# Kernel tuning notes

Measured on AMD Instinct MI355X. Metric: run time of the kernel, lower is better.

## Reference

```python
import jax, jax.numpy as jnp
import numpy as np

B, T, C = 2, 2048, 2048
H, KV, D = 16, 4, 128   # n_head, n_kv_head, head_dim
EPS = 1.1920929e-07     # torch.finfo(float32).eps, F.rms_norm default


def setup_inputs() -> dict:
    key = jax.random.key(0)
    ks = jax.random.split(key, 7)
    x = jax.random.normal(ks[0], (B, T, C), dtype=jnp.float32)
    # rope angles: cos/sin of positions, broadcastable to [B,T,H,D//2]
    inv_freq = 1.0 / (10000.0 ** (jnp.arange(0, D // 2, dtype=jnp.float32) / (D // 2)))
    ang = jnp.arange(T, dtype=jnp.float32)[:, None] * inv_freq[None, :]
    cos = jnp.cos(ang)[None, :, None, :]  # [1,T,1,D/2]
    sin = jnp.sin(ang)[None, :, None, :]
    s = 0.02
    Wq = jax.random.normal(ks[1], (C, H * D), dtype=jnp.float32) * s
    Wk = jax.random.normal(ks[2], (C, KV * D), dtype=jnp.float32) * s
    Wv = jax.random.normal(ks[3], (C, KV * D), dtype=jnp.float32) * s
    Wo = jax.random.normal(ks[4], (C, C), dtype=jnp.float32) * s
    return {"x": x, "cos": cos, "sin": sin, "Wq": Wq, "Wk": Wk, "Wv": Wv, "Wo": Wo}


def _rope(t, cos, sin):
    d = t.shape[-1] // 2
    t1, t2 = t[..., :d], t[..., d:]
    return jnp.concatenate([t1 * cos + t2 * sin, -t1 * sin + t2 * cos], axis=-1)


def _rmsnorm(t):
    return t * jax.lax.rsqrt(jnp.mean(t * t, axis=-1, keepdims=True) + EPS)


def reference(x, cos, sin, Wq, Wk, Wv, Wo):
    q = (x @ Wq).reshape(B, T, H, D)
    k = (x @ Wk).reshape(B, T, KV, D)
    v = (x @ Wv).reshape(B, T, KV, D)
    q = _rmsnorm(_rope(q, cos, sin))
    k = _rmsnorm(_rope(k, cos, sin))
    # [B, KV, G, T, D] query grouped per kv head (GQA)
    G = H // KV
    qh = q.transpose(0, 2, 1, 3).reshape(B, KV, G, T, D)
    kh = k.transpose(0, 2, 1, 3)  # [B, KV, T, D]
    vh = v.transpose(0, 2, 1, 3)
    scale = 1.0 / np.sqrt(D).astype(np.float32)
    scores = jnp.einsum('bhgqd,bhkd->bhgqk', qh, kh) * scale
    causal = jnp.tril(jnp.ones((T, T), dtype=bool))
    scores = jnp.where(causal, scores, jnp.finfo(scores.dtype).min)
    attn = jax.nn.softmax(scores, axis=-1)
    y = jnp.einsum('bhgqk,bhkd->bhgqd', attn, vh)  # [B,KV,G,T,D]
    y = y.reshape(B, H, T, D).transpose(0, 2, 1, 3).reshape(B, T, C)
    return y @ Wo
```

## Files before the change

kernel.cpp:

```cpp
#include <hip/hip_runtime.h>

using bf16x8 = __attribute__((ext_vector_type(8))) short;
using f32x4  = __attribute__((ext_vector_type(4))) float;

#define B_  2
#define T_  2048
#define C_  2048
#define H_  16
#define KV_ 4
#define D_  128

__device__ __forceinline__ unsigned short f2b(float f) {
  union { float f; unsigned int u; } v; v.f = f;
  unsigned int r = v.u + 0x7fffu + ((v.u >> 16) & 1u);
  return (unsigned short)(r >> 16);
}
__device__ __forceinline__ float b2f(unsigned short u) {
  union { unsigned int u; float f; } v; v.u = ((unsigned int)u) << 16;
  return v.f;
}
__device__ __forceinline__ unsigned int cvt_pk_bf16(float lo, float hi) {
  unsigned int r;
  asm("v_cvt_pk_bf16_f32 %0, %1, %2" : "=v"(r) : "v"(lo), "v"(hi));
  return r;
}
__device__ __forceinline__ void gld_lds16(const void* g, void* l) {
  __builtin_amdgcn_global_load_lds(
      (__attribute__((address_space(1))) void*)g,
      (__attribute__((address_space(3))) void*)l, 16, 0, 0);
}

__global__ void cast_bf16_k(const float* __restrict__ in, unsigned short* __restrict__ out) {
  int i = blockIdx.x * 256 + threadIdx.x;
  float4 f = ((const float4*)in)[i];
  ushort4 u; u.x = f2b(f.x); u.y = f2b(f.y); u.z = f2b(f.z); u.w = f2b(f.w);
  ((ushort4*)out)[i] = u;
}

__global__ void wtrans4(const float* __restrict__ Wq, const float* __restrict__ Wk,
                        const float* __restrict__ Wv, const float* __restrict__ Wo,
                        unsigned short* __restrict__ Wqt, unsigned short* __restrict__ Wkt,
                        unsigned short* __restrict__ Wvt, unsigned short* __restrict__ Wot) {
  __shared__ float s[32][33];
  int id = blockIdx.x;
  const float* W; unsigned short* Wt; int N;
  if (id < 4096)      { W = Wq; Wt = Wqt; N = 2048; }
  else if (id < 5120) { W = Wk; Wt = Wkt; N = 512;  id -= 4096; }
  else if (id < 6144) { W = Wv; Wt = Wvt; N = 512;  id -= 5120; }
  else                { W = Wo; Wt = Wot; N = 2048; id -= 6144; }
  int ntiles = N >> 5;
  int n0 = (id % ntiles) * 32, k0 = (id / ntiles) * 32;
  int tx = threadIdx.x, ty = threadIdx.y;
  #pragma unroll
  for (int yy = 0; yy < 32; yy += 8)
    s[ty + yy][tx] = W[(size_t)(k0 + ty + yy) * N + n0 + tx];
  __syncthreads();
  #pragma unroll
  for (int yy = 0; yy < 32; yy += 8)
    Wt[(size_t)(n0 + ty + yy) * 2048 + k0 + tx] = f2b(s[tx][ty + yy]);
}

template <bool OUT_BF16>
__device__ __forceinline__ void gemm_tile(
    const unsigned short* __restrict__ A, const unsigned short* __restrict__ Bt,
    void* __restrict__ Cv, int K, int ldc, int m0, int n0b, int n0c,
    unsigned short* sA, unsigned short* sB)
{
  const int tid  = threadIdx.x;
  const int lane = tid & 63, w = tid >> 6;
  const int quad = lane >> 4, l16 = lane & 15;
  const int wm = (w >> 1) * 64, wn = (w & 1) * 64;

  f32x4 acc[4][4] = {};

  const unsigned short* Abase = A  + (size_t)m0  * K;
  const unsigned short* Bbase = Bt + (size_t)n0b * K;

  for (int k0 = 0; k0 < K; k0 += 32) {
    #pragma unroll
    for (int r = 0; r < 2; ++r) {
      int c = tid + r * 256;
      int row = c >> 2, col = (c & 3) * 8;
      gld_lds16(Abase + (size_t)row * K + k0 + col, sA + c * 8);
      gld_lds16(Bbase + (size_t)row * K + k0 + col, sB + c * 8);
    }
    __syncthreads();
    bf16x8 af[4], bfr[4];
    #pragma unroll
    for (int i = 0; i < 4; ++i)
      af[i]  = *(const bf16x8*)(sA + (wm + i * 16 + l16) * 32 + quad * 8);
    #pragma unroll
    for (int j = 0; j < 4; ++j)
      bfr[j] = *(const bf16x8*)(sB + (wn + j * 16 + l16) * 32 + quad * 8);
    #pragma unroll
    for (int i = 0; i < 4; ++i)
      #pragma unroll
      for (int j = 0; j < 4; ++j)
        acc[i][j] = __builtin_amdgcn_mfma_f32_16x16x32_bf16(af[i], bfr[j], acc[i][j], 0, 0, 0);
    __syncthreads();
  }
  #pragma unroll
  for (int i = 0; i < 4; ++i) {
    #pragma unroll
    for (int r = 0; r < 4; ++r) {
      int row = m0 + wm + i * 16 + quad * 4 + r;
      #pragma unroll
      for (int j = 0; j < 4; ++j) {
        int col = n0c + wn + j * 16 + l16;
        float v = acc[i][j][r];
        if (OUT_BF16) ((unsigned short*)Cv)[(size_t)row * ldc + col] = f2b(v);
        else          ((float*)Cv)[(size_t)row * ldc + col] = v;
      }
    }
  }
}

__global__ void out_gemm(const unsigned short* __restrict__ yb,
                         const unsigned short* __restrict__ Wot,
                         float* __restrict__ out) {
  __shared__ unsigned short sA[128 * 32], sB[128 * 32];
  gemm_tile<false>(yb, Wot, out, C_, C_, blockIdx.y * 128, blockIdx.x * 128, blockIdx.x * 128,
                   sA, sB);
}

__global__ __launch_bounds__(512, 2) void qkv_gemm2p(
    const unsigned short* __restrict__ xb,
    const unsigned short* __restrict__ Wt,
    unsigned short* __restrict__ qkv) {
  __shared__ unsigned short lds[57344];

  const int id  = (int)blockIdx.x;
  const int xcd = id & 7, j = id >> 3;
  const int mt  = xcd * 2 + (j >> 4);
  const int nt  = j & 15;
  const int m0 = mt * 256, n0 = nt * 192;

  const int tid = (int)threadIdx.x;
  const int w = tid >> 6, lane = tid & 63;
  const int quad = lane >> 4, l16 = lane & 15;
  const int wr = w >> 1, wc = w & 1;
  const int swz = (l16 & 12) << 1;

  const unsigned short* Ab = xb + (size_t)m0 * 2048;
  const unsigned short* Bb = Wt + (size_t)n0 * 2048;

  int ar[4], axc[4];
  #pragma unroll
  for (int kq = 0; kq < 4; ++kq) {
    int ca = tid + kq * 512;
    ar[kq]  = (ca & 1023) >> 2;
    axc[kq] = ((ca & 3) * 8) ^ ((((ca & 1023) >> 4) & 3) << 3);
  }
  const int khb1 = (tid < 256) ? 0 : 1;
  int bidx[3] = { tid, tid + 512 - khb1 * 768, tid + 256 };
  int bkh[3]  = { 0, khb1, 1 };
  int br[3], bxc[3];
  #pragma unroll
  for (int kq = 0; kq < 3; ++kq) {
    br[kq]  = bidx[kq] >> 2;
    bxc[kq] = ((bidx[kq] & 3) * 8) ^ (((bidx[kq] >> 4) & 3) << 3);
  }

#define STAGE(buf, kb) do { \
    unsigned short* da_ = lds + (buf) * 16384; \
    _Pragma("unroll") \
    for (int kq = 0; kq < 4; ++kq) { \
      int ca_ = tid + kq * 512; \
      gld_lds16(Ab + (size_t)ar[kq] * 2048 + (kb) + (ca_ >> 10) * 32 + axc[kq], da_ + ca_ * 8); \
    } \
    unsigned short* db_ = lds + 32768 + (buf) * 12288; \
    _Pragma("unroll") \
    for (int kq = 0; kq < 3; ++kq) \
      gld_lds16(Bb + (size_t)br[kq] * 2048 + (kb) + bkh[kq] * 32 + bxc[kq], \
                db_ + bkh[kq] * 6144 + bidx[kq] * 8); \
  } while (0)

  f32x4 acc[4][6] = {};

  STAGE(0, 0);
  __syncthreads();

  const unsigned short* aB = lds + (wr * 64 + l16) * 32 + (quad * 8 ^ swz);
  const unsigned short* bB = lds + 32768 + (wc * 96 + l16) * 32 + (quad * 8 ^ swz);

  for (int t = 0; t < 32; ++t) {
    const int cur = t & 1;
    if (t < 31) STAGE(cur ^ 1, (t + 1) * 64);
    #pragma unroll
    for (int kh = 0; kh < 2; ++kh) {
      bf16x8 a[4], b[6];
      #pragma unroll
      for (int m = 0; m < 4; ++m)
        a[m] = *(const bf16x8*)(aB + cur * 16384 + kh * 8192 + m * 512);
      #pragma unroll
      for (int n = 0; n < 6; ++n)
        b[n] = *(const bf16x8*)(bB + cur * 12288 + kh * 6144 + n * 512);
      #pragma unroll
      for (int m = 0; m < 4; ++m)
        #pragma unroll
        for (int n = 0; n < 6; ++n)
          acc[m][n] = __builtin_amdgcn_mfma_f32_16x16x32_bf16(a[m], b[n], acc[m][n], 0, 0, 0);
    }
    __syncthreads();
  }
#undef STAGE

  #pragma unroll
  for (int m = 0; m < 4; ++m)
    #pragma unroll
    for (int r = 0; r < 4; ++r) {
      int row = m0 + wr * 64 + m * 16 + quad * 4 + r;
      #pragma unroll
      for (int n = 0; n < 6; ++n) {
        int col = n0 + wc * 96 + n * 16 + l16;
        qkv[(size_t)row * 3072 + col] = f2b(acc[m][n][r]);
      }
    }
}

template <int NH>
__global__ void ropenorm(const unsigned short* __restrict__ in,
                         const float* __restrict__ cs, const float* __restrict__ sn,
                         unsigned short* __restrict__ out, float oscale, int ld, int off) {
  int row  = blockIdx.x * 4 + (threadIdx.x >> 6);
  int lane = threadIdx.x & 63;
  int head = row % NH;
  int t = (row / NH) & (T_ - 1);
  int b = row / (NH * T_);
  const unsigned short* p = in + (size_t)(b * T_ + t) * ld + off + head * D_;
  unsigned int u  = *(const unsigned int*)(p + 2 * lane);
  unsigned int up = (unsigned int)__shfl_xor((int)u, 32, 64);
  int dh = (lane & 31) * 2;
  float2 c2 = ((const float2*)(cs + t * 64))[lane & 31];
  float2 s2 = ((const float2*)(sn + t * 64))[lane & 31];
  float a0 = b2f((unsigned short)(u & 0xffff)),  a1 = b2f((unsigned short)(u >> 16));
  float p0 = b2f((unsigned short)(up & 0xffff)), p1 = b2f((unsigned short)(up >> 16));
  float sgn = (lane < 32) ? 1.0f : -1.0f;
  float oa = a0 * c2.x + sgn * p0 * s2.x;
  float ob = a1 * c2.y + sgn * p1 * s2.y;
  float ss = oa * oa + ob * ob;
  #pragma unroll
  for (int off2 = 32; off2 > 0; off2 >>= 1) ss += __shfl_xor(ss, off2, 64);
  float r = rsqrtf(ss * (1.0f / 128.0f) + 1.1920929e-07f) * oscale;
  unsigned int outu = cvt_pk_bf16(oa * r, ob * r);
  size_t base = ((size_t)((b * NH + head) * 128 + (t >> 4))) * 2048 + (size_t)(t & 15) * 8;
  int f = ((lane < 32) ? 0 : 8) + (dh >> 3);
  *(unsigned int*)(out + base + (size_t)f * 128 + (dh & 7)) = outu;
}

__global__ void vfrag_k(const unsigned short* __restrict__ qkv, unsigned short* __restrict__ vf) {
  int it = blockIdx.x;
  int b = blockIdx.y >> 2, kv = blockIdx.y & 3;
  int d = threadIdx.x, ty = threadIdx.y;
  int t0 = it * 64;
  size_t obase = ((size_t)((b * KV_ + kv) * 32 + it)) * 8192
               + (size_t)(d >> 4) * 1024 + (size_t)(d & 15) * 8;
  #pragma unroll
  for (int tcg = 0; tcg < 4; ++tcg) {
    int tc = ty * 4 + tcg;
    unsigned short val[8];
    #pragma unroll
    for (int e = 0; e < 8; ++e)
      val[e] = qkv[((size_t)(b * T_) + t0 + tc * 8 + e) * 3072 + 2560 + kv * D_ + d];
    ushort4 u0 = {val[0], val[1], val[2], val[3]};
    ushort4 u1 = {val[4], val[5], val[6], val[7]};
    *(ushort4*)(vf + obase + (size_t)tc * 128)     = u0;
    *(ushort4*)(vf + obase + (size_t)tc * 128 + 4) = u1;
  }
}

__global__ __launch_bounds__(512, 2) void attn_kernel(
    const unsigned short* __restrict__ qf, const unsigned short* __restrict__ kf,
    const unsigned short* __restrict__ vf, unsigned short* __restrict__ yb) {
  __shared__ __align__(16) char smem[135168];
  unsigned short* kls = (unsigned short*)smem;
  unsigned short* vls = (unsigned short*)(smem + 65536);
  unsigned short* Pls = (unsigned short*)(smem + 98304);

  const int xp = (int)blockIdx.x, b = xp >> 2, kv = xp & 3;
  const int jy = (int)blockIdx.y;
  const int tid = (int)threadIdx.x;
  const int w = tid >> 6, lane = tid & 63;
  const int quad = lane >> 4, l16 = lane & 15;
  const int hh = w & 3, half = w >> 2;
  const int h = kv * 4 + hh;
  unsigned short* myP = Pls + w * (32 * 72);

  const unsigned short* Kf = kf + (size_t)(b * KV_ + kv) * 128 * 2048;
  const unsigned short* Vf = vf + (size_t)(b * KV_ + kv) * 32 * 8192;

  const int swl = quad << 4;
  const int cs0 = (tid * 8) ^ swl;
  const int cs1 = ((tid + 512) * 8) ^ swl;
  const int cd0 = tid * 8, cd1 = tid * 8 + 4096;

#define STAGE_K(buf, it0) do { \
    const unsigned short* s_ = Kf + (size_t)(it0) * 8192; \
    unsigned short* d_ = kls + (buf) * 16384; \
    gld_lds16(s_ + cs0, d_ + cd0);               gld_lds16(s_ + cs1, d_ + cd1); \
    gld_lds16(s_ + 8192 + cs0, d_ + 8192 + cd0); gld_lds16(s_ + 8192 + cs1, d_ + 8192 + cd1); \
  } while (0)
#define STAGE_V(it0) do { \
    const unsigned short* s_ = Vf + (size_t)(it0) * 8192; \
    gld_lds16(s_ + cs0, vls + cd0);               gld_lds16(s_ + cs1, vls + cd1); \
    gld_lds16(s_ + 8192 + cs0, vls + 8192 + cd0); gld_lds16(s_ + 8192 + cs1, vls + 8192 + cd1); \
  } while (0)

  for (int ph = 0; ph < 2; ++ph) {
    const int qt = ph ? (63 - jy) : jy;
    const int q0 = qt * 32;
    const int ntile = (qt >> 1) + 1;
    const int R = (ntile + 1) >> 1;

    const unsigned short* Qf = qf + ((size_t)(b * H_ + h) * 128 + qt * 2) * 2048;
    bf16x8 bq[2][4];
    #pragma unroll
    for (int i = 0; i < 2; ++i)
      #pragma unroll
      for (int kk = 0; kk < 4; ++kk)
        bq[i][kk] = *(const bf16x8*)(Qf + (size_t)i * 2048 + (kk * 4 + quad) * 128 + l16 * 8);

    float l_i[2] = {0.f, 0.f};
    f32x4 o[2][8] = {};

    STAGE_K(0, 0);

    for (int r = 0; r < R; ++r) {
      const int cur = r & 1;
      const bool more = (r + 1 < R);
      STAGE_V(2 * r);
      if (more) STAGE_K(cur ^ 1, 2 * r + 2);
      if (more) asm volatile("s_waitcnt vmcnt(8)" ::: "memory");
      else      asm volatile("s_waitcnt vmcnt(4)" ::: "memory");
      __builtin_amdgcn_s_barrier();

      const int it = 2 * r + half;
      const bool active = it < ntile;
      f32x4 sc[4][2] = {};
      if (active) {
        const unsigned short* kb = kls + cur * 16384 + half * 8192;
        #pragma unroll
        for (int kk = 0; kk < 4; ++kk) {
          bf16x8 ak[4];
          #pragma unroll
          for (int jt = 0; jt < 4; ++jt)
            ak[jt] = *(const bf16x8*)(kb + ((jt * 2048 + (kk * 4 + quad) * 128 + l16 * 8) ^ swl));
          #pragma unroll
          for (int jt = 0; jt < 4; ++jt)
            #pragma unroll
            for (int i = 0; i < 2; ++i)
              sc[jt][i] = __builtin_amdgcn_mfma_f32_16x16x32_bf16(ak[jt], bq[i][kk], sc[jt][i], 0, 0, 0);
        }
        if (it == ntile - 1) {
          #pragma unroll
          for (int jt = 0; jt < 4; ++jt) {
            int kg = it * 64 + jt * 16 + quad * 4;
            #pragma unroll
            for (int i = 0; i < 2; ++i) {
              int qg = q0 + i * 16 + l16;
              #pragma unroll
              for (int rr = 0; rr < 4; ++rr)
                if (kg + rr > qg) sc[jt][i][rr] = -3.0e38f;
            }
          }
        }
        #pragma unroll
        for (int i = 0; i < 2; ++i) {
          float part = 0.f;
          #pragma unroll
          for (int jt = 0; jt < 4; ++jt)
            #pragma unroll
            for (int rr = 0; rr < 4; ++rr) {
              float p = __expf(sc[jt][i][rr] - 12.0f);
              sc[jt][i][rr] = p; part += p;
            }
          l_i[i] += part;
        }
        #pragma unroll
        for (int i = 0; i < 2; ++i)
          #pragma unroll
          for (int jt = 0; jt < 4; ++jt) {
            uint2 uu;
            uu.x = cvt_pk_bf16(sc[jt][i][0], sc[jt][i][1]);
            uu.y = cvt_pk_bf16(sc[jt][i][2], sc[jt][i][3]);
            *(uint2*)(myP + (i * 16 + l16) * 72 + jt * 16 + quad * 4) = uu;
          }
      }

      if (more) asm volatile("s_waitcnt vmcnt(4)" ::: "memory");
      else      asm volatile("s_waitcnt vmcnt(0)" ::: "memory");
      __builtin_amdgcn_s_barrier();

      if (active) {
        const unsigned short* vb = vls + half * 8192;
        #pragma unroll
        for (int kk2 = 0; kk2 < 2; ++kk2) {
          bf16x8 ap[2], bv2[8];
          #pragma unroll
          for (int i = 0; i < 2; ++i)
            ap[i] = *(const bf16x8*)(myP + (i * 16 + l16) * 72 + kk2 * 32 + quad * 8);
          #pragma unroll
          for (int jj = 0; jj < 8; ++jj)
            bv2[jj] = *(const bf16x8*)(vb + ((jj * 1024 + (kk2 * 4 + quad) * 128 + l16 * 8) ^ swl));
          #pragma unroll
          for (int i = 0; i < 2; ++i)
            #pragma unroll
            for (int jj = 0; jj < 8; ++jj)
              o[i][jj] = __builtin_amdgcn_mfma_f32_16x16x32_bf16(ap[i], bv2[jj], o[i][jj], 0, 0, 0);
        }
      }
      __builtin_amdgcn_s_barrier();
    }

    float lsum[2];
    #pragma unroll
    for (int i = 0; i < 2; ++i) {
      float l = l_i[i];
      l += __shfl_xor(l, 16, 64);
      l += __shfl_xor(l, 32, 64);
      lsum[i] = l;
    }

    __syncthreads();
    float* oc = (float*)smem + hh * 4256;
    float* lc = oc + 32 * 132;
    if (half == 1) {
      #pragma unroll
      for (int i = 0; i < 2; ++i) {
        if (quad == 0) lc[i * 16 + l16] = lsum[i];
        #pragma unroll
        for (int jj = 0; jj < 8; ++jj)
          #pragma unroll
          for (int rr = 0; rr < 4; ++rr)
            oc[(i * 16 + quad * 4 + rr) * 132 + jj * 16 + l16] = o[i][jj][rr];
      }
    }
    __syncthreads();
    if (half == 0) {
      #pragma unroll
      for (int i = 0; i < 2; ++i) {
        float l = lsum[i] + lc[i * 16 + l16];
        float linv = 1.0f / l;
        float lr[4];
        #pragma unroll
        for (int rr = 0; rr < 4; ++rr) lr[rr] = __shfl(linv, quad * 4 + rr, 64);
        #pragma unroll
        for (int rr = 0; rr < 4; ++rr) {
          int tg = q0 + i * 16 + quad * 4 + rr;
          unsigned short* yr = yb + (((size_t)(b * T_ + tg)) * H_ + h) * D_;
          #pragma unroll
          for (int jj = 0; jj < 8; ++jj) {
            float vsum = o[i][jj][rr] + oc[(i * 16 + quad * 4 + rr) * 132 + jj * 16 + l16];
            yr[jj * 16 + l16] = f2b(vsum * lr[rr]);
          }
        }
      }
    }
    __syncthreads();
  }
#undef STAGE_K
#undef STAGE_V
}

extern "C" void kernel_launch(void* const* d_in, const int* in_sizes, int n_in,
                              void* d_out, int out_size, void* d_ws, size_t ws_size,
                              hipStream_t stream) {
  (void)in_sizes; (void)n_in; (void)out_size; (void)ws_size;
  const float* x  = (const float*)d_in[0];
  const float* cs = (const float*)d_in[1];
  const float* sn = (const float*)d_in[2];
  const float* Wq = (const float*)d_in[3];
  const float* Wk = (const float*)d_in[4];
  const float* Wv = (const float*)d_in[5];
  const float* Wo = (const float*)d_in[6];
  float* out = (float*)d_out;
  char* ws = (char*)d_ws;

  unsigned short* xb     = (unsigned short*)(ws + 0);
  unsigned short* Wqkvt  = (unsigned short*)(ws + 16777216);
  unsigned short* Wot    = (unsigned short*)(ws + 29360128);
  unsigned short* qkvcat = (unsigned short*)(ws + 37748736);
  unsigned short* qfr    = (unsigned short*)(ws + 62914560);
  unsigned short* kfr    = (unsigned short*)(ws + 79691776);
  unsigned short* vfr    = (unsigned short*)(ws + 83886080);
  unsigned short* yb     = xb;

  cast_bf16_k<<<dim3(8192), dim3(256), 0, stream>>>(x, xb);
  wtrans4<<<dim3(10240), dim3(32, 8), 0, stream>>>(
      Wq, Wk, Wv, Wo,
      Wqkvt, Wqkvt + (size_t)2048 * 2048, Wqkvt + (size_t)2560 * 2048, Wot);
  qkv_gemm2p<<<dim3(256), dim3(512), 0, stream>>>(xb, Wqkvt, qkvcat);
  ropenorm<16><<<dim3(16384), dim3(256), 0, stream>>>(qkvcat, cs, sn, qfr,
                                                      0.08838834764831845f, 3072, 0);
  ropenorm<4><<<dim3(4096),  dim3(256), 0, stream>>>(qkvcat, cs, sn, kfr, 1.0f, 3072, 2048);
  vfrag_k<<<dim3(32, 8), dim3(128, 2), 0, stream>>>(qkvcat, vfr);
  attn_kernel<<<dim3(8, 32), dim3(512), 0, stream>>>(qfr, kfr, vfr, yb);
  out_gemm<<<dim3(16, 32), dim3(256), 0, stream>>>(yb, Wot, out);
}
```

Baseline: 294.2 us.

## Merge prep and rope launches, replace output GEMM with double-buffered kernel

Folds the x cast and the weight transposes into one prep launch, and merges the Q and K rope/norm launches into one. It also replaces the simple 128x128 output GEMM with a 256x128-tile, 512-thread kernel that double-buffers LDS, uses a swizzled layout and maps blocks to XCDs. The aim is to cut launch overhead and make the output projection more efficient, at the cost of more LDS per block and fewer blocks in the output GEMM.

```diff
diff --git a/kernel.cpp b/kernel.cpp
--- a/kernel.cpp
+++ b/kernel.cpp
@@ -30,19 +30,21 @@
       (__attribute__((address_space(3))) void*)l, 16, 0, 0);
 }
 
-__global__ void cast_bf16_k(const float* __restrict__ in, unsigned short* __restrict__ out) {
-  int i = blockIdx.x * 256 + threadIdx.x;
-  float4 f = ((const float4*)in)[i];
-  ushort4 u; u.x = f2b(f.x); u.y = f2b(f.y); u.z = f2b(f.z); u.w = f2b(f.w);
-  ((ushort4*)out)[i] = u;
-}
-
-__global__ void wtrans4(const float* __restrict__ Wq, const float* __restrict__ Wk,
-                        const float* __restrict__ Wv, const float* __restrict__ Wo,
-                        unsigned short* __restrict__ Wqt, unsigned short* __restrict__ Wkt,
-                        unsigned short* __restrict__ Wvt, unsigned short* __restrict__ Wot) {
+__global__ void prep(const float* __restrict__ x, unsigned short* __restrict__ xb,
+                     const float* __restrict__ Wq, const float* __restrict__ Wk,
+                     const float* __restrict__ Wv, const float* __restrict__ Wo,
+                     unsigned short* __restrict__ Wqt, unsigned short* __restrict__ Wkt,
+                     unsigned short* __restrict__ Wvt, unsigned short* __restrict__ Wot) {
   __shared__ float s[32][33];
-  int id = blockIdx.x;
+  int bid = blockIdx.x, tid = threadIdx.x;
+  if (bid < 8192) {
+    int i = bid * 256 + tid;
+    float4 f = ((const float4*)x)[i];
+    ushort4 u; u.x = f2b(f.x); u.y = f2b(f.y); u.z = f2b(f.z); u.w = f2b(f.w);
+    ((ushort4*)xb)[i] = u;
+    return;
+  }
+  int id = bid - 8192;
   const float* W; unsigned short* Wt; int N;
   if (id < 4096)      { W = Wq; Wt = Wqt; N = 2048; }
   else if (id < 5120) { W = Wk; Wt = Wkt; N = 512;  id -= 4096; }
@@ -50,7 +52,7 @@
   else                { W = Wo; Wt = Wot; N = 2048; id -= 6144; }
   int ntiles = N >> 5;
   int n0 = (id % ntiles) * 32, k0 = (id / ntiles) * 32;
-  int tx = threadIdx.x, ty = threadIdx.y;
+  int tx = tid & 31, ty = tid >> 5;
   #pragma unroll
   for (int yy = 0; yy < 32; yy += 8)
     s[ty + yy][tx] = W[(size_t)(k0 + ty + yy) * N + n0 + tx];
@@ -58,69 +60,6 @@
   #pragma unroll
   for (int yy = 0; yy < 32; yy += 8)
     Wt[(size_t)(n0 + ty + yy) * 2048 + k0 + tx] = f2b(s[tx][ty + yy]);
-}
-
-template <bool OUT_BF16>
-__device__ __forceinline__ void gemm_tile(
-    const unsigned short* __restrict__ A, const unsigned short* __restrict__ Bt,
-    void* __restrict__ Cv, int K, int ldc, int m0, int n0b, int n0c,
-    unsigned short* sA, unsigned short* sB)
-{
-  const int tid  = threadIdx.x;
-  const int lane = tid & 63, w = tid >> 6;
-  const int quad = lane >> 4, l16 = lane & 15;
-  const int wm = (w >> 1) * 64, wn = (w & 1) * 64;
-
-  f32x4 acc[4][4] = {};
-
-  const unsigned short* Abase = A  + (size_t)m0  * K;
-  const unsigned short* Bbase = Bt + (size_t)n0b * K;
-
-  for (int k0 = 0; k0 < K; k0 += 32) {
-    #pragma unroll
-    for (int r = 0; r < 2; ++r) {
-      int c = tid + r * 256;
-      int row = c >> 2, col = (c & 3) * 8;
-      gld_lds16(Abase + (size_t)row * K + k0 + col, sA + c * 8);
-      gld_lds16(Bbase + (size_t)row * K + k0 + col, sB + c * 8);
-    }
-    __syncthreads();
-    bf16x8 af[4], bfr[4];
-    #pragma unroll
-    for (int i = 0; i < 4; ++i)
-      af[i]  = *(const bf16x8*)(sA + (wm + i * 16 + l16) * 32 + quad * 8);
-    #pragma unroll
-    for (int j = 0; j < 4; ++j)
-      bfr[j] = *(const bf16x8*)(sB + (wn + j * 16 + l16) * 32 + quad * 8);
-    #pragma unroll
-    for (int i = 0; i < 4; ++i)
-      #pragma unroll
-      for (int j = 0; j < 4; ++j)
-        acc[i][j] = __builtin_amdgcn_mfma_f32_16x16x32_bf16(af[i], bfr[j], acc[i][j], 0, 0, 0);
-    __syncthreads();
-  }
-  #pragma unroll
-  for (int i = 0; i < 4; ++i) {
-    #pragma unroll
-    for (int r = 0; r < 4; ++r) {
-      int row = m0 + wm + i * 16 + quad * 4 + r;
-      #pragma unroll
-      for (int j = 0; j < 4; ++j) {
-        int col = n0c + wn + j * 16 + l16;
-        float v = acc[i][j][r];
-        if (OUT_BF16) ((unsigned short*)Cv)[(size_t)row * ldc + col] = f2b(v);
-        else          ((float*)Cv)[(size_t)row * ldc + col] = v;
-      }
-    }
-  }
-}
-
-__global__ void out_gemm(const unsigned short* __restrict__ yb,
-                         const unsigned short* __restrict__ Wot,
-                         float* __restrict__ out) {
-  __shared__ unsigned short sA[128 * 32], sB[128 * 32];
-  gemm_tile<false>(yb, Wot, out, C_, C_, blockIdx.y * 128, blockIdx.x * 128, blockIdx.x * 128,
-                   sA, sB);
 }
 
 __global__ __launch_bounds__(512, 2) void qkv_gemm2p(
@@ -218,16 +157,109 @@
     }
 }
 
+__global__ __launch_bounds__(512, 2) void out_gemm2p(
+    const unsigned short* __restrict__ yb,
+    const unsigned short* __restrict__ Wot,
+    float* __restrict__ out) {
+  __shared__ unsigned short lds[49152];
+
+  const int id  = (int)blockIdx.x;
+  const int xcd = id & 7, j = id >> 3;
+  const int mt  = xcd * 2 + (j >> 4);
+  const int nt  = j & 15;
+  const int m0 = mt * 256, n0 = nt * 128;
+
+  const int tid = (int)threadIdx.x;
+  const int w = tid >> 6, lane = tid & 63;
+  const int quad = lane >> 4, l16 = lane & 15;
+  const int wr = w >> 1, wc = w & 1;
+  const int swz = (l16 & 12) << 1;
+
+  const unsigned short* Ab = yb  + (size_t)m0 * 2048;
+  const unsigned short* Bb = Wot + (size_t)n0 * 2048;
+
+  int ar[4], axc[4];
+  #pragma unroll
+  for (int kq = 0; kq < 4; ++kq) {
+    int ca = tid + kq * 512;
+    ar[kq]  = (ca & 1023) >> 2;
+    axc[kq] = ((ca & 3) * 8) ^ ((((ca & 1023) >> 4) & 3) << 3);
+  }
+  int brr[2], bxc[2];
+  #pragma unroll
+  for (int kq = 0; kq < 2; ++kq) {
+    int cb = tid + kq * 512;
+    brr[kq] = (cb & 511) >> 2;
+    bxc[kq] = ((cb & 3) * 8) ^ ((((cb & 511) >> 4) & 3) << 3);
+  }
+
+#define STAGE(buf, kb) do { \
+    unsigned short* da_ = lds + (buf) * 16384; \
+    _Pragma("unroll") \
+    for (int kq = 0; kq < 4; ++kq) { \
+      int ca_ = tid + kq * 512; \
+      gld_lds16(Ab + (size_t)ar[kq] * 2048 + (kb) + (ca_ >> 10) * 32 + axc[kq], da_ + ca_ * 8); \
+    } \
+    unsigned short* db_ = lds + 32768 + (buf) * 8192; \
+    _Pragma("unroll") \
+    for (int kq = 0; kq < 2; ++kq) { \
+      int cb_ = tid + kq * 512; \
+      gld_lds16(Bb + (size_t)brr[kq] * 2048 + (kb) + kq * 32 + bxc[kq], db_ + cb_ * 8); \
+    } \
+  } while (0)
+
+  f32x4 acc[4][4] = {};
+
+  STAGE(0, 0);
+  __syncthreads();
+
+  const unsigned short* aB = lds + (wr * 64 + l16) * 32 + (quad * 8 ^ swz);
+  const unsigned short* bB = lds + 32768 + (wc * 64 + l16) * 32 + (quad * 8 ^ swz);
+
+  for (int t = 0; t < 32; ++t) {
+    const int cur = t & 1;
+    if (t < 31) STAGE(cur ^ 1, (t + 1) * 64);
+    #pragma unroll
+    for (int kh = 0; kh < 2; ++kh) {
+      bf16x8 a[4], b[4];
+      #pragma unroll
+      for (int m = 0; m < 4; ++m)
+        a[m] = *(const bf16x8*)(aB + cur * 16384 + kh * 8192 + m * 512);
+      #pragma unroll
+      for (int n = 0; n < 4; ++n)
+        b[n] = *(const bf16x8*)(bB + cur * 8192 + kh * 4096 + n * 512);
+      #pragma unroll
+      for (int m = 0; m < 4; ++m)
+        #pragma unroll
+        for (int n = 0; n < 4; ++n)
+          acc[m][n] = __builtin_amdgcn_mfma_f32_16x16x32_bf16(a[m], b[n], acc[m][n], 0, 0, 0);
+    }
+    __syncthreads();
+  }
+#undef STAGE
+
+  #pragma unroll
+  for (int m = 0; m < 4; ++m)
+    #pragma unroll
+    for (int r = 0; r < 4; ++r) {
+      int row = m0 + wr * 64 + m * 16 + quad * 4 + r;
+      #pragma unroll
+      for (int n = 0; n < 4; ++n) {
+        int col = n0 + wc * 64 + n * 16 + l16;
+        out[(size_t)row * 2048 + col] = acc[m][n][r];
+      }
+    }
+}
+
 template <int NH>
-__global__ void ropenorm(const unsigned short* __restrict__ in,
-                         const float* __restrict__ cs, const float* __restrict__ sn,
-                         unsigned short* __restrict__ out, float oscale, int ld, int off) {
-  int row  = blockIdx.x * 4 + (threadIdx.x >> 6);
-  int lane = threadIdx.x & 63;
+__device__ __forceinline__ void ropenorm_row(
+    const unsigned short* __restrict__ in, const float* __restrict__ cs,
+    const float* __restrict__ sn, unsigned short* __restrict__ out,
+    float oscale, int off, int row, int lane) {
   int head = row % NH;
   int t = (row / NH) & (T_ - 1);
   int b = row / (NH * T_);
-  const unsigned short* p = in + (size_t)(b * T_ + t) * ld + off + head * D_;
+  const unsigned short* p = in + (size_t)(b * T_ + t) * 3072 + off + head * D_;
   unsigned int u  = *(const unsigned int*)(p + 2 * lane);
   unsigned int up = (unsigned int)__shfl_xor((int)u, 32, 64);
   int dh = (lane & 31) * 2;
@@ -246,6 +278,20 @@
   size_t base = ((size_t)((b * NH + head) * 128 + (t >> 4))) * 2048 + (size_t)(t & 15) * 8;
   int f = ((lane < 32) ? 0 : 8) + (dh >> 3);
   *(unsigned int*)(out + base + (size_t)f * 128 + (dh & 7)) = outu;
+}
+
+__global__ void ropenorm_qk(const unsigned short* __restrict__ qkv,
+                            const float* __restrict__ cs, const float* __restrict__ sn,
+                            unsigned short* __restrict__ qfr,
+                            unsigned short* __restrict__ kfr) {
+  int bid = blockIdx.x;
+  int lane = threadIdx.x & 63;
+  int wv = threadIdx.x >> 6;
+  if (bid < 16384) {
+    ropenorm_row<16>(qkv, cs, sn, qfr, 0.08838834764831845f, 0, bid * 4 + wv, lane);
+  } else {
+    ropenorm_row<4>(qkv, cs, sn, kfr, 1.0f, 2048, (bid - 16384) * 4 + wv, lane);
+  }
 }
 
 __global__ void vfrag_k(const unsigned short* __restrict__ qkv, unsigned short* __restrict__ vf) {
@@ -485,15 +531,12 @@
   unsigned short* vfr    = (unsigned short*)(ws + 83886080);
   unsigned short* yb     = xb;
 
-  cast_bf16_k<<<dim3(8192), dim3(256), 0, stream>>>(x, xb);
-  wtrans4<<<dim3(10240), dim3(32, 8), 0, stream>>>(
-      Wq, Wk, Wv, Wo,
+  prep<<<dim3(18432), dim3(256), 0, stream>>>(
+      x, xb, Wq, Wk, Wv, Wo,
       Wqkvt, Wqkvt + (size_t)2048 * 2048, Wqkvt + (size_t)2560 * 2048, Wot);
   qkv_gemm2p<<<dim3(256), dim3(512), 0, stream>>>(xb, Wqkvt, qkvcat);
-  ropenorm<16><<<dim3(16384), dim3(256), 0, stream>>>(qkvcat, cs, sn, qfr,
-                                                      0.08838834764831845f, 3072, 0);
-  ropenorm<4><<<dim3(4096),  dim3(256), 0, stream>>>(qkvcat, cs, sn, kfr, 1.0f, 3072, 2048);
+  ropenorm_qk<<<dim3(20480), dim3(256), 0, stream>>>(qkvcat, cs, sn, qfr, kfr);
   vfrag_k<<<dim3(32, 8), dim3(128, 2), 0, stream>>>(qkvcat, vfr);
   attn_kernel<<<dim3(8, 32), dim3(512), 0, stream>>>(qfr, kfr, vfr, yb);
-  out_gemm<<<dim3(16, 32), dim3(256), 0, stream>>>(yb, Wot, out);
-}
+  out_gemm2p<<<dim3(256), dim3(512), 0, stream>>>(yb, Wot, out);
+}
```

Measured after the change: 282.1 us. -4.1%, faster.
